# Performance work log

Measured on AMD Instinct MI355X. Metric: run time of the kernel, lower is better.

The kernel has to match this reference:

```python
import jax, jax.numpy as jnp
import numpy as np

IN_CHANNELS = 64
OUT_CHANNELS = 64
MODES = 64


def setup_inputs() -> dict:
    key = jax.random.key(0)
    kq, kk, kv = jax.random.split(key, 3)
    B, L, E, H = 16, 2048, 64, 8
    S = 2048
    q = jax.random.normal(kq, (B, L, E, H), dtype=jnp.float32)
    k = jax.random.normal(kk, (B, S, E, H), dtype=jnp.float32)
    v = jax.random.normal(kv, (B, S, E, H), dtype=jnp.float32)
    return {"q": q, "k": k, "v": v}


def reference(q, k, v):
    # q: [B,L,E,H], k/v: [B,S,E,H]. v is unused (matches the source module).
    B, L, E, H = q.shape
    S = k.shape[1]
    Mq = min(L // 2, MODES)
    Mkv = min(S // 2, MODES)

    xq = jnp.transpose(q, (0, 3, 2, 1))  # [B,H,E,L]
    xk = jnp.transpose(k, (0, 3, 2, 1))  # [B,H,E,S]

    # rFFT along time, keep lowest Mq/Mkv modes (index_q/index_kv are range(...))
    xq_ft = jnp.fft.rfft(xq, axis=-1)[..., :Mq]    # [B,H,E,Mq] complex64
    xk_ft = jnp.fft.rfft(xk, axis=-1)[..., :Mkv]   # [B,H,E,Mkv]

    # compl_mul1d is a plain complex multiply inside einsum (no conjugate)
    xqk_ft = jnp.einsum('bhex,bhey->bhxy', xq_ft, xk_ft)  # [B,H,Mq,Mkv]

    # tanh applied separately to real and imaginary parts
    xqk_ft = jax.lax.complex(jnp.tanh(xqk_ft.real), jnp.tanh(xqk_ft.imag))

    xqkv_ft = jnp.einsum('bhxy,bhey->bhex', xqk_ft, xk_ft)  # [B,H,E,Mq]

    # scatter selected modes into zero spectrum, then inverse FFT
    out_ft = jnp.zeros((B, H, E, L // 2 + 1), dtype=jnp.complex64)
    out_ft = out_ft.at[..., :Mq].set(xqkv_ft)
    scale = jnp.float32(IN_CHANNELS * OUT_CHANNELS)
    out = jnp.fft.irfft(out_ft / scale, n=L, axis=-1)  # [B,H,E,L] real
    return jnp.transpose(out, (0, 3, 1, 2))  # [B,L,H,E]
```

## Files before the change

### kernel.cpp

```cpp
#include <hip/hip_runtime.h>
#include <math.h>

typedef __attribute__((ext_vector_type(8))) short short8v;
typedef __attribute__((ext_vector_type(16))) float f32x16;

#define BF_U 0
#define BI_U 262144
#define XP_F 270336
#define YT_U 17317888

__device__ inline unsigned short bf16_rne(float x) {
    unsigned int u = __float_as_uint(x);
    u += 0x7FFFu + ((u >> 16) & 1u);
    return (unsigned short)(u >> 16);
}
__device__ inline float bf16_f(unsigned short h) {
    return __uint_as_float(((unsigned int)h) << 16);
}

__global__ __launch_bounds__(256) void basis_kernel(float* __restrict__ w) {
    int idx = blockIdx.x * 256 + threadIdx.x;
    const float th = 0.0030679615757712823f;
    unsigned short* bw = (unsigned short*)w;
    if (idx < 65536) {
        int t = idx >> 6, m = idx & 63;
        int j = (m * t) & 2047;
        float s, c; sincosf(th * (float)j, &s, &c);
        float ns = -s;
        int cc = t >> 4, kh = (t >> 3) & 1, e = t & 7;
        int base = BF_U + cc * 4096 + kh * 512 + m * 8 + e;
        unsigned short chv = bf16_rne(c), shv = bf16_rne(ns);
        bw[base]        = chv;
        bw[base + 1024] = bf16_rne(c - bf16_f(chv));
        bw[base + 2048] = shv;
        bw[base + 3072] = bf16_rne(ns - bf16_f(shv));
    }
    if (idx < 69632) {
        int m = idx / 1088, t = idx - m * 1088;
        int j = (m * t) & 2047;
        float s, c; sincosf(th * (float)j, &s, &c);
        int slab = m >> 4, kh = (m >> 3) & 1, e = m & 7;
        int base = BI_U + (slab * 8 + kh) * 8704 + t * 8 + e;
        unsigned short chv = bf16_rne(c), shv = bf16_rne(s);
        bw[base]         = chv;
        bw[base + 17408] = bf16_rne(c - bf16_f(chv));
        bw[base + 34816] = shv;
        bw[base + 52224] = bf16_rne(s - bf16_f(shv));
    }
}

__global__ __launch_bounds__(256, 4) void fdft_kernel(const float* __restrict__ q,
                                                      const float* __restrict__ k,
                                                      float* __restrict__ ws) {
    const int chtile = blockIdx.x;
    const int b      = blockIdx.y;
    const int zz     = blockIdx.z >> 1;
    const int mgrp   = blockIdx.z & 1;
    const int part   = zz & 3;
    const float* __restrict__ src = (zz >> 2) ? k : q;
    const unsigned short* __restrict__ basisF = (const unsigned short*)ws + BF_U;
    float* __restrict__ xp = ws + XP_F + (size_t)(zz * 16 + b) * 65536;

    __shared__ __align__(16) unsigned short lds[2][8192];

    const int tid  = threadIdx.x;
    const int lane = tid & 63;
    const int wc   = tid >> 6;
    const int ml   = lane & 31;
    const int khl  = lane >> 5;

    const int chl = tid & 127;
    const int kh  = tid >> 7;
    const float* __restrict__ ap = src + (size_t)b * 2048 * 512 + chtile * 128 + chl;

    f32x16 accR, accI;
#pragma unroll
    for (int i = 0; i < 16; ++i) { accR[i] = 0.f; accI[i] = 0.f; }

    float av[8], pv[8];

    auto LOAD = [&](int s) {
        const int t0 = part * 256 + s * 16 + kh * 8;
#pragma unroll
        for (int e = 0; e < 8; ++e) {
            int t = t0 + e;
            int pr = (t == 0) ? 1024 : 2048 - t;
            av[e] = ap[(size_t)t * 512];
            pv[e] = ap[(size_t)pr * 512];
        }
    };
    auto WRITE = [&](int bf) {
        unsigned short* D = &lds[bf][0];
        short8v xu, xl, xv, xw;
#pragma unroll
        for (int e = 0; e < 8; ++e) {
            float u = av[e] + pv[e], v = av[e] - pv[e];
            unsigned short uh = bf16_rne(u); unsigned short vh = bf16_rne(v);
            xu[e] = (short)uh; xl[e] = (short)bf16_rne(u - bf16_f(uh));
            xv[e] = (short)vh; xw[e] = (short)bf16_rne(v - bf16_f(vh));
        }
        const int doff = kh * 1024 + chl * 8;
        *(short8v*)(D + doff)        = xu;
        *(short8v*)(D + doff + 2048) = xl;
        *(short8v*)(D + doff + 4096) = xv;
        *(short8v*)(D + doff + 6144) = xw;
    };
    auto COMP = [&](int bf, int s) {
        const unsigned short* bb = basisF + (part * 16 + s) * 4096
                                 + khl * 512 + (mgrp * 32 + ml) * 8;
        short8v cH = *(const short8v*)(bb);
        short8v cL = *(const short8v*)(bb + 1024);
        short8v sH = *(const short8v*)(bb + 2048);
        short8v sL = *(const short8v*)(bb + 3072);
        const unsigned short* L = &lds[bf][0];
        const int b0 = khl * 1024 + (wc * 32 + ml) * 8;
        short8v uH = *(const short8v*)(L + b0);
        short8v uL = *(const short8v*)(L + b0 + 2048);
        short8v vH = *(const short8v*)(L + b0 + 4096);
        short8v vL = *(const short8v*)(L + b0 + 6144);
        accR = __builtin_amdgcn_mfma_f32_32x32x16_bf16(cH, uH, accR, 0, 0, 0);
        accR = __builtin_amdgcn_mfma_f32_32x32x16_bf16(cH, uL, accR, 0, 0, 0);
        accR = __builtin_amdgcn_mfma_f32_32x32x16_bf16(cL, uH, accR, 0, 0, 0);
        accI = __builtin_amdgcn_mfma_f32_32x32x16_bf16(sH, vH, accI, 0, 0, 0);
        accI = __builtin_amdgcn_mfma_f32_32x32x16_bf16(sH, vL, accI, 0, 0, 0);
        accI = __builtin_amdgcn_mfma_f32_32x32x16_bf16(sL, vH, accI, 0, 0, 0);
    };

    LOAD(0); WRITE(0); __syncthreads();
    for (int s = 0; s < 16; ++s) {
        if (s < 15) LOAD(s + 1);
        COMP(s & 1, s);
        if (s < 15) { WRITE((s + 1) & 1); __syncthreads(); }
    }

    if (part == 0) {
        float a0 = src[(size_t)b * 2048 * 512 + (size_t)1024 * 512
                       + chtile * 128 + wc * 32 + ml];
#pragma unroll
        for (int reg = 1; reg < 16; reg += 2) accR[reg] -= 2.f * a0;
    }

    float* LF = (float*)(&lds[0][0]);
#pragma unroll 1
    for (int pass = 0; pass < 2; ++pass) {
        __syncthreads();
#pragma unroll
        for (int reg = 0; reg < 16; ++reg) {
            const int mL = (reg & 3) + 8 * (reg >> 2) + 4 * khl;
            LF[mL * 129 + wc * 32 + ml] = pass ? accI[reg] : accR[reg];
        }
        __syncthreads();
#pragma unroll
        for (int u8 = 0; u8 < 4; ++u8) {
            int unit = tid + u8 * 256;
            int e4 = unit & 3, h = (unit >> 2) & 7, mL = unit >> 5;
            float4 val;
            val.x = LF[mL * 129 + ((e4 * 4 + 0) * 8 + h)];
            val.y = LF[mL * 129 + ((e4 * 4 + 1) * 8 + h)];
            val.z = LF[mL * 129 + ((e4 * 4 + 2) * 8 + h)];
            val.w = LF[mL * 129 + ((e4 * 4 + 3) * 8 + h)];
            *(float4*)&xp[pass * 32768 + (h * 64 + mgrp * 32 + mL) * 64
                          + chtile * 16 + e4 * 4] = val;
        }
    }
}

__global__ __launch_bounds__(256) void mid_kernel(float* __restrict__ ws) {
    const int h = blockIdx.x, b = blockIdx.y, xh = blockIdx.z;
    unsigned short* __restrict__ YTb = (unsigned short*)ws + YT_U + (size_t)b * 131072;

    __shared__ float Qs[2][32][64];
    __shared__ float Ksw[2][64][64];

    const int tid = threadIdx.x;
    for (int slot = tid; slot < 1024; slot += 256) {
        int p = slot >> 9, ml = (slot >> 4) & 31, c4 = slot & 15;
        int off = ((p * 8 + h) * 64 + xh * 32 + ml) * 64 + c4 * 4;
        float4 acc = make_float4(0.f, 0.f, 0.f, 0.f);
#pragma unroll
        for (int part = 0; part < 4; ++part) {
            const float4 v = *(const float4*)(ws + XP_F + (size_t)(part * 16 + b) * 65536 + off);
            acc.x += v.x; acc.y += v.y; acc.z += v.z; acc.w += v.w;
        }
        *(float4*)(&Qs[p][ml][c4 * 4]) = acc;
    }
    for (int slot = tid; slot < 2048; slot += 256) {
        int p = slot >> 10, ml = (slot >> 4) & 63, c4 = slot & 15;
        int off = ((p * 8 + h) * 64 + ml) * 64 + c4 * 4;
        float4 acc = make_float4(0.f, 0.f, 0.f, 0.f);
#pragma unroll
        for (int part = 0; part < 4; ++part) {
            const float4 v = *(const float4*)(ws + XP_F + (size_t)((4 + part) * 16 + b) * 65536 + off);
            acc.x += v.x; acc.y += v.y; acc.z += v.z; acc.w += v.w;
        }
        Ksw[p][ml][(c4 * 4 + 0) ^ ml] = acc.x;
        Ksw[p][ml][(c4 * 4 + 1) ^ ml] = acc.y;
        Ksw[p][ml][(c4 * 4 + 2) ^ ml] = acc.z;
        Ksw[p][ml][(c4 * 4 + 3) ^ ml] = acc.w;
    }
    __syncthreads();

    const int lane = tid & 63;
    const int wid  = tid >> 6;
    const int xb   = wid * 8;

    float sr[8], si[8];
#pragma unroll
    for (int i = 0; i < 8; ++i) { sr[i] = 0.f; si[i] = 0.f; }
    const int y = lane;
    for (int e = 0; e < 64; ++e) {
        float kr = Ksw[0][y][e ^ y];
        float ki = Ksw[1][y][e ^ y];
#pragma unroll
        for (int i = 0; i < 8; ++i) {
            float qr = Qs[0][xb + i][e];
            float qi = Qs[1][xb + i][e];
            sr[i] += qr * kr; sr[i] -= qi * ki;
            si[i] += qr * ki; si[i] += qi * kr;
        }
    }
    float tr[8], ti[8];
#pragma unroll
    for (int i = 0; i < 8; ++i) { tr[i] = tanhf(sr[i]); ti[i] = tanhf(si[i]); }
    __syncthreads();
#pragma unroll
    for (int i = 0; i < 8; ++i) {
        Qs[0][xb + i][y] = tr[i];
        Qs[1][xb + i][y] = ti[i];
    }
    __syncthreads();

    float vr[8], vi[8];
#pragma unroll
    for (int i = 0; i < 8; ++i) { vr[i] = 0.f; vi[i] = 0.f; }
    const int e = lane;
    for (int yy = 0; yy < 64; ++yy) {
        float kr = Ksw[0][yy][e ^ yy];
        float ki = Ksw[1][yy][e ^ yy];
#pragma unroll
        for (int i = 0; i < 8; ++i) {
            float trr = Qs[0][xb + i][yy];
            float tii = Qs[1][xb + i][yy];
            vr[i] += trr * kr; vr[i] -= tii * ki;
            vi[i] += trr * ki; vi[i] += tii * kr;
        }
    }
#pragma unroll
    for (int i = 0; i < 8; ++i) {
        int x = xh * 32 + xb + i;
        float f = (x == 0 ? 1.0f : 2.0f) * (1.0f / (2048.0f * 4096.0f));
        float yr = f * vr[i];
        float yi = -f * vi[i];
        int off = (h * 64 + e) * 64 + x;
        unsigned short rH = bf16_rne(yr), iH = bf16_rne(yi);
        YTb[off]         = rH;
        YTb[32768 + off] = bf16_rne(yr - bf16_f(rH));
        YTb[65536 + off] = iH;
        YTb[98304 + off] = bf16_rne(yi - bf16_f(iH));
    }
}

__global__ __launch_bounds__(256, 3) void idft_kernel(const float* __restrict__ ws,
                                                      float* __restrict__ out) {
    const int tt0    = blockIdx.x * 64;
    const int chtile = blockIdx.y;
    const int b      = blockIdx.z;
    const unsigned short* __restrict__ basisI = (const unsigned short*)ws + BI_U;
    const unsigned short* __restrict__ YTb = (const unsigned short*)ws + YT_U + (size_t)b * 131072;

    __shared__ __align__(16) unsigned short ldsY[2][12288];

    const int tid  = threadIdx.x;
    const int lane = tid & 63;
    const int wv   = tid >> 6;
    const int wt   = wv >> 1, wcc = wv & 1;
    const int ml   = lane & 31;
    const int khl  = lane >> 5;

    f32x16 accP0, accP1, accQ0, accQ1;
#pragma unroll
    for (int i = 0; i < 16; ++i) { accP0[i] = 0.f; accP1[i] = 0.f; accQ0[i] = 0.f; accQ1[i] = 0.f; }

    const int tblA = tid >> 7;
    const int chlA = tid & 127;
    short8v sA0, sA1, sB0, sB1;

    auto LOAD = [&](int s) {
        const unsigned short* gA = YTb + tblA * 32768 + (chtile * 128 + chlA) * 64 + s * 16;
        const unsigned short* gB = gA + 2 * 32768;
        sA0 = *(const short8v*)(gA);
        sA1 = *(const short8v*)(gA + 8);
        sB0 = *(const short8v*)(gB);
        sB1 = *(const short8v*)(gB + 8);
    };
    auto WRITE = [&](int bf) {
        unsigned short* D = &ldsY[bf][0];
        const int offA = tblA * 3072 + chlA * 24;
        *(short8v*)(D + offA)            = sA0;
        *(short8v*)(D + offA + 8)        = sA1;
        *(short8v*)(D + offA + 2 * 3072)     = sB0;
        *(short8v*)(D + offA + 2 * 3072 + 8) = sB1;
    };
    auto COMP = [&](int bf, int s) {
        const unsigned short* bb = basisI + (s * 8 + khl) * 8704 + (tt0 + wt * 32 + ml) * 8;
        short8v cH = *(const short8v*)(bb);
        short8v cL = *(const short8v*)(bb + 17408);
        short8v sH = *(const short8v*)(bb + 34816);
        short8v sL = *(const short8v*)(bb + 52224);
        const unsigned short* L = &ldsY[bf][0];
        const int b0 = (wcc * 64 + ml) * 24 + khl * 8;
        short8v yrH0 = *(const short8v*)(L + b0);
        short8v yrL0 = *(const short8v*)(L + 3072 + b0);
        short8v yiH0 = *(const short8v*)(L + 6144 + b0);
        short8v yiL0 = *(const short8v*)(L + 9216 + b0);
        const int b1 = b0 + 32 * 24;
        short8v yrH1 = *(const short8v*)(L + b1);
        short8v yrL1 = *(const short8v*)(L + 3072 + b1);
        short8v yiH1 = *(const short8v*)(L + 6144 + b1);
        short8v yiL1 = *(const short8v*)(L + 9216 + b1);
        accP0 = __builtin_amdgcn_mfma_f32_32x32x16_bf16(cH, yrH0, accP0, 0, 0, 0);
        accP0 = __builtin_amdgcn_mfma_f32_32x32x16_bf16(cH, yrL0, accP0, 0, 0, 0);
        accP0 = __builtin_amdgcn_mfma_f32_32x32x16_bf16(cL, yrH0, accP0, 0, 0, 0);
        accQ0 = __builtin_amdgcn_mfma_f32_32x32x16_bf16(sH, yiH0, accQ0, 0, 0, 0);
        accQ0 = __builtin_amdgcn_mfma_f32_32x32x16_bf16(sH, yiL0, accQ0, 0, 0, 0);
        accQ0 = __builtin_amdgcn_mfma_f32_32x32x16_bf16(sL, yiH0, accQ0, 0, 0, 0);
        accP1 = __builtin_amdgcn_mfma_f32_32x32x16_bf16(cH, yrH1, accP1, 0, 0, 0);
        accP1 = __builtin_amdgcn_mfma_f32_32x32x16_bf16(cH, yrL1, accP1, 0, 0, 0);
        accP1 = __builtin_amdgcn_mfma_f32_32x32x16_bf16(cL, yrH1, accP1, 0, 0, 0);
        accQ1 = __builtin_amdgcn_mfma_f32_32x32x16_bf16(sH, yiH1, accQ1, 0, 0, 0);
        accQ1 = __builtin_amdgcn_mfma_f32_32x32x16_bf16(sH, yiL1, accQ1, 0, 0, 0);
        accQ1 = __builtin_amdgcn_mfma_f32_32x32x16_bf16(sL, yiH1, accQ1, 0, 0, 0);
    };

    LOAD(0); WRITE(0); __syncthreads();
    for (int s = 0; s < 4; ++s) {
        if (s < 3) LOAD(s + 1);
        COMP(s & 1, s);
        if (s < 3) { WRITE((s + 1) & 1); __syncthreads(); }
    }

    float* __restrict__ ob = out + (size_t)b * 2048 * 512;
#pragma unroll
    for (int reg = 0; reg < 16; ++reg) {
        const int tL = wt * 32 + (reg & 3) + 8 * (reg >> 2) + 4 * khl;
        const int t  = tt0 + tL;
        const int ch0 = chtile * 128 + wcc * 64 + ml;
        float p0 = accP0[reg], q0 = accQ0[reg];
        float p1 = accP1[reg], q1 = accQ1[reg];
        if (t <= 1024) {
            ob[(size_t)t * 512 + ch0]      = p0 + q0;
            ob[(size_t)t * 512 + ch0 + 32] = p1 + q1;
        }
        if (t >= 1 && t <= 1023) {
            ob[(size_t)(2048 - t) * 512 + ch0]      = p0 - q0;
            ob[(size_t)(2048 - t) * 512 + ch0 + 32] = p1 - q1;
        }
    }
}

extern "C" void kernel_launch(void* const* d_in, const int* in_sizes, int n_in,
                              void* d_out, int out_size, void* d_ws, size_t ws_size,
                              hipStream_t stream) {
    const float* q = (const float*)d_in[0];
    const float* k = (const float*)d_in[1];
    float* ws = (float*)d_ws;
    float* out = (float*)d_out;

    hipLaunchKernelGGL(basis_kernel, dim3(272), dim3(256), 0, stream, ws);
    hipLaunchKernelGGL(fdft_kernel, dim3(4, 16, 16), dim3(256), 0, stream, q, k, ws);
    hipLaunchKernelGGL(mid_kernel, dim3(8, 16, 2), dim3(256), 0, stream, ws);
    hipLaunchKernelGGL(idft_kernel, dim3(17, 4, 16), dim3(256), 0, stream, ws, out);
}
```

Measured before the change: 95.25 us.

## Merge mode groups in forward DFT block and stage basis through LDS

The forward DFT kernel now computes all 64 modes per block instead of splitting them across two blocks along grid z. Each wave computes a 32-mode by 64-channel tile with two accumulator pairs, so the q/k time samples are loaded from global memory and bf16-split once rather than twice. The basis tile is also loaded cooperatively into LDS instead of being read per-wave from global. In exchange, grid size halves, LDS grows, register pressure rises, and the launch bound drops to 2 blocks per CU, which may reduce latency hiding.

Result: faster. 87.87 us, median of 2 (-7.7%).

```diff
diff --git a/kernel.cpp b/kernel.cpp
--- a/kernel.cpp
+++ b/kernel.cpp
@@ -49,23 +49,23 @@
     }
 }
 
-__global__ __launch_bounds__(256, 4) void fdft_kernel(const float* __restrict__ q,
+__global__ __launch_bounds__(256, 2) void fdft_kernel(const float* __restrict__ q,
                                                       const float* __restrict__ k,
                                                       float* __restrict__ ws) {
     const int chtile = blockIdx.x;
     const int b      = blockIdx.y;
-    const int zz     = blockIdx.z >> 1;
-    const int mgrp   = blockIdx.z & 1;
-    const int part   = zz & 3;
-    const float* __restrict__ src = (zz >> 2) ? k : q;
+    const int z      = blockIdx.z;
+    const int part   = z & 3;
+    const float* __restrict__ src = (z >> 2) ? k : q;
     const unsigned short* __restrict__ basisF = (const unsigned short*)ws + BF_U;
-    float* __restrict__ xp = ws + XP_F + (size_t)(zz * 16 + b) * 65536;
-
-    __shared__ __align__(16) unsigned short lds[2][8192];
+    float* __restrict__ xp = ws + XP_F + (size_t)(z * 16 + b) * 65536;
+
+    __shared__ __align__(16) unsigned short lds[2][12288];
 
     const int tid  = threadIdx.x;
     const int lane = tid & 63;
-    const int wc   = tid >> 6;
+    const int wv   = tid >> 6;
+    const int wm   = wv >> 1, wc = wv & 1;
     const int ml   = lane & 31;
     const int khl  = lane >> 5;
 
@@ -73,11 +73,12 @@
     const int kh  = tid >> 7;
     const float* __restrict__ ap = src + (size_t)b * 2048 * 512 + chtile * 128 + chl;
 
-    f32x16 accR, accI;
-#pragma unroll
-    for (int i = 0; i < 16; ++i) { accR[i] = 0.f; accI[i] = 0.f; }
+    f32x16 accR0, accR1, accI0, accI1;
+#pragma unroll
+    for (int i = 0; i < 16; ++i) { accR0[i] = 0.f; accR1[i] = 0.f; accI0[i] = 0.f; accI1[i] = 0.f; }
 
     float av[8], pv[8];
+    short8v bas0, bas1;
 
     auto LOAD = [&](int s) {
         const int t0 = part * 256 + s * 16 + kh * 8;
@@ -88,9 +89,14 @@
             av[e] = ap[(size_t)t * 512];
             pv[e] = ap[(size_t)pr * 512];
         }
+        const unsigned short* bsrc = basisF + (size_t)(part * 16 + s) * 4096;
+        bas0 = *(const short8v*)(bsrc + tid * 8);
+        bas1 = *(const short8v*)(bsrc + 2048 + tid * 8);
     };
     auto WRITE = [&](int bf) {
         unsigned short* D = &lds[bf][0];
+        *(short8v*)(D + tid * 8)        = bas0;
+        *(short8v*)(D + 2048 + tid * 8) = bas1;
         short8v xu, xl, xv, xw;
 #pragma unroll
         for (int e = 0; e < 8; ++e) {
@@ -99,45 +105,55 @@
             xu[e] = (short)uh; xl[e] = (short)bf16_rne(u - bf16_f(uh));
             xv[e] = (short)vh; xw[e] = (short)bf16_rne(v - bf16_f(vh));
         }
-        const int doff = kh * 1024 + chl * 8;
+        const int doff = 4096 + (kh * 128 + chl) * 8;
         *(short8v*)(D + doff)        = xu;
         *(short8v*)(D + doff + 2048) = xl;
         *(short8v*)(D + doff + 4096) = xv;
         *(short8v*)(D + doff + 6144) = xw;
     };
-    auto COMP = [&](int bf, int s) {
-        const unsigned short* bb = basisF + (part * 16 + s) * 4096
-                                 + khl * 512 + (mgrp * 32 + ml) * 8;
-        short8v cH = *(const short8v*)(bb);
-        short8v cL = *(const short8v*)(bb + 1024);
-        short8v sH = *(const short8v*)(bb + 2048);
-        short8v sL = *(const short8v*)(bb + 3072);
+    auto COMP = [&](int bf) {
         const unsigned short* L = &lds[bf][0];
-        const int b0 = khl * 1024 + (wc * 32 + ml) * 8;
-        short8v uH = *(const short8v*)(L + b0);
-        short8v uL = *(const short8v*)(L + b0 + 2048);
-        short8v vH = *(const short8v*)(L + b0 + 4096);
-        short8v vL = *(const short8v*)(L + b0 + 6144);
-        accR = __builtin_amdgcn_mfma_f32_32x32x16_bf16(cH, uH, accR, 0, 0, 0);
-        accR = __builtin_amdgcn_mfma_f32_32x32x16_bf16(cH, uL, accR, 0, 0, 0);
-        accR = __builtin_amdgcn_mfma_f32_32x32x16_bf16(cL, uH, accR, 0, 0, 0);
-        accI = __builtin_amdgcn_mfma_f32_32x32x16_bf16(sH, vH, accI, 0, 0, 0);
-        accI = __builtin_amdgcn_mfma_f32_32x32x16_bf16(sH, vL, accI, 0, 0, 0);
-        accI = __builtin_amdgcn_mfma_f32_32x32x16_bf16(sL, vH, accI, 0, 0, 0);
+        const int aoff = (khl * 64 + wm * 32 + ml) * 8;
+        short8v cH = *(const short8v*)(L + aoff);
+        short8v cL = *(const short8v*)(L + 1024 + aoff);
+        short8v sH = *(const short8v*)(L + 2048 + aoff);
+        short8v sL = *(const short8v*)(L + 3072 + aoff);
+        const int b0 = 4096 + (khl * 128 + wc * 64 + ml) * 8;
+        short8v uH0 = *(const short8v*)(L + b0);
+        short8v uL0 = *(const short8v*)(L + b0 + 2048);
+        short8v vH0 = *(const short8v*)(L + b0 + 4096);
+        short8v vL0 = *(const short8v*)(L + b0 + 6144);
+        short8v uH1 = *(const short8v*)(L + b0 + 256);
+        short8v uL1 = *(const short8v*)(L + b0 + 256 + 2048);
+        short8v vH1 = *(const short8v*)(L + b0 + 256 + 4096);
+        short8v vL1 = *(const short8v*)(L + b0 + 256 + 6144);
+        accR0 = __builtin_amdgcn_mfma_f32_32x32x16_bf16(cH, uH0, accR0, 0, 0, 0);
+        accR0 = __builtin_amdgcn_mfma_f32_32x32x16_bf16(cH, uL0, accR0, 0, 0, 0);
+        accR0 = __builtin_amdgcn_mfma_f32_32x32x16_bf16(cL, uH0, accR0, 0, 0, 0);
+        accI0 = __builtin_amdgcn_mfma_f32_32x32x16_bf16(sH, vH0, accI0, 0, 0, 0);
+        accI0 = __builtin_amdgcn_mfma_f32_32x32x16_bf16(sH, vL0, accI0, 0, 0, 0);
+        accI0 = __builtin_amdgcn_mfma_f32_32x32x16_bf16(sL, vH0, accI0, 0, 0, 0);
+        accR1 = __builtin_amdgcn_mfma_f32_32x32x16_bf16(cH, uH1, accR1, 0, 0, 0);
+        accR1 = __builtin_amdgcn_mfma_f32_32x32x16_bf16(cH, uL1, accR1, 0, 0, 0);
+        accR1 = __builtin_amdgcn_mfma_f32_32x32x16_bf16(cL, uH1, accR1, 0, 0, 0);
+        accI1 = __builtin_amdgcn_mfma_f32_32x32x16_bf16(sH, vH1, accI1, 0, 0, 0);
+        accI1 = __builtin_amdgcn_mfma_f32_32x32x16_bf16(sH, vL1, accI1, 0, 0, 0);
+        accI1 = __builtin_amdgcn_mfma_f32_32x32x16_bf16(sL, vH1, accI1, 0, 0, 0);
     };
 
     LOAD(0); WRITE(0); __syncthreads();
     for (int s = 0; s < 16; ++s) {
         if (s < 15) LOAD(s + 1);
-        COMP(s & 1, s);
+        COMP(s & 1);
         if (s < 15) { WRITE((s + 1) & 1); __syncthreads(); }
     }
 
     if (part == 0) {
-        float a0 = src[(size_t)b * 2048 * 512 + (size_t)1024 * 512
-                       + chtile * 128 + wc * 32 + ml];
-#pragma unroll
-        for (int reg = 1; reg < 16; reg += 2) accR[reg] -= 2.f * a0;
+        const size_t b1024 = (size_t)b * 2048 * 512 + (size_t)1024 * 512 + chtile * 128;
+        float a0 = src[b1024 + wc * 64 + ml];
+        float a1 = src[b1024 + wc * 64 + 32 + ml];
+#pragma unroll
+        for (int reg = 1; reg < 16; reg += 2) { accR0[reg] -= 2.f * a0; accR1[reg] -= 2.f * a1; }
     }
 
     float* LF = (float*)(&lds[0][0]);
@@ -146,21 +162,22 @@
         __syncthreads();
 #pragma unroll
         for (int reg = 0; reg < 16; ++reg) {
-            const int mL = (reg & 3) + 8 * (reg >> 2) + 4 * khl;
-            LF[mL * 129 + wc * 32 + ml] = pass ? accI[reg] : accR[reg];
+            const int m = wm * 32 + (reg & 3) + 8 * (reg >> 2) + 4 * khl;
+            const int c0l = wc * 64 + ml;
+            LF[m * 129 + c0l]      = pass ? accI0[reg] : accR0[reg];
+            LF[m * 129 + c0l + 32] = pass ? accI1[reg] : accR1[reg];
         }
         __syncthreads();
 #pragma unroll
-        for (int u8 = 0; u8 < 4; ++u8) {
+        for (int u8 = 0; u8 < 8; ++u8) {
             int unit = tid + u8 * 256;
-            int e4 = unit & 3, h = (unit >> 2) & 7, mL = unit >> 5;
+            int e4 = unit & 3, h = (unit >> 2) & 7, m = unit >> 5;
             float4 val;
-            val.x = LF[mL * 129 + ((e4 * 4 + 0) * 8 + h)];
-            val.y = LF[mL * 129 + ((e4 * 4 + 1) * 8 + h)];
-            val.z = LF[mL * 129 + ((e4 * 4 + 2) * 8 + h)];
-            val.w = LF[mL * 129 + ((e4 * 4 + 3) * 8 + h)];
-            *(float4*)&xp[pass * 32768 + (h * 64 + mgrp * 32 + mL) * 64
-                          + chtile * 16 + e4 * 4] = val;
+            val.x = LF[m * 129 + ((e4 * 4 + 0) * 8 + h)];
+            val.y = LF[m * 129 + ((e4 * 4 + 1) * 8 + h)];
+            val.z = LF[m * 129 + ((e4 * 4 + 2) * 8 + h)];
+            val.w = LF[m * 129 + ((e4 * 4 + 3) * 8 + h)];
+            *(float4*)&xp[pass * 32768 + (h * 64 + m) * 64 + chtile * 16 + e4 * 4] = val;
         }
     }
 }
@@ -367,7 +384,7 @@
     float* out = (float*)d_out;
 
     hipLaunchKernelGGL(basis_kernel, dim3(272), dim3(256), 0, stream, ws);
-    hipLaunchKernelGGL(fdft_kernel, dim3(4, 16, 16), dim3(256), 0, stream, q, k, ws);
+    hipLaunchKernelGGL(fdft_kernel, dim3(4, 16, 8), dim3(256), 0, stream, q, k, ws);
     hipLaunchKernelGGL(mid_kernel, dim3(8, 16, 2), dim3(256), 0, stream, ws);
     hipLaunchKernelGGL(idft_kernel, dim3(17, 4, 16), dim3(256), 0, stream, ws, out);
 }
```
